# Optimization experiments

Measured on AMD Instinct MI355X. Metric: run time of the kernel, lower is better.

Reference implementation:

```python
import jax, jax.numpy as jnp
import numpy as np

K = 7           # kernel_size
GROUPS = 16     # channels // group_channels = 256 // 16
GC = 16         # group_channels
BN_EPS = 1e-5


def setup_inputs() -> dict:
    key = jax.random.key(0)
    ks = jax.random.split(key, 6)
    B, C, H, W = 4, 256, 64, 64
    cr = C // 4                      # reduction_ratio = 4
    k2g = K * K * GROUPS             # conv2 out channels = 784
    return {
        "feature_map": jax.random.normal(ks[0], (B, C, H, W), jnp.float32),
        "guide_map":   jax.random.normal(ks[1], (B, C, H, W), jnp.float32),
        "w1": jax.random.normal(ks[2], (cr, C), jnp.float32) * 0.05,
        "bn_gamma": jnp.ones((cr,), jnp.float32),
        "bn_beta":  jnp.zeros((cr,), jnp.float32),
        "bn_mean":  jax.random.normal(ks[3], (cr,), jnp.float32) * 0.1,
        "bn_var":   jax.random.uniform(ks[4], (cr,), jnp.float32, 0.5, 1.5),
        "w2": jax.random.normal(ks[5], (k2g, cr), jnp.float32) * 0.05,
        "b2": jnp.zeros((k2g,), jnp.float32),
    }


def reference(feature_map, guide_map, w1, bn_gamma, bn_beta, bn_mean, bn_var, w2, b2):
    b, c, h, w = feature_map.shape
    # conv1 (1x1) + BN (inference stats) + ReLU
    x = jnp.einsum("oc,bchw->bohw", w1, guide_map)
    inv = bn_gamma / jnp.sqrt(bn_var + BN_EPS)
    x = x * inv[None, :, None, None] + (bn_beta - bn_mean * inv)[None, :, None, None]
    x = jax.nn.relu(x)
    # conv2 (1x1): dynamic per-pixel kernel weights -> [b, groups, k^2, h, w]
    weight = jnp.einsum("oc,bchw->bohw", w2, x) + b2[None, :, None, None]
    weight = weight.reshape(b, GROUPS, K * K, h, w)
    # unfold feature_map (same padding, stride 1) -> [b, c, k^2, h, w]
    pad = (K - 1) // 2
    fp = jnp.pad(feature_map, ((0, 0), (0, 0), (pad, pad), (pad, pad)))
    patches = jnp.stack(
        [fp[:, :, i:i + h, j:j + w] for i in range(K) for j in range(K)], axis=2
    )
    patches = patches.reshape(b, GROUPS, GC, K * K, h, w)
    # dynamic weighted aggregation over kernel positions, then residual
    out = jnp.einsum("bgkhw,bgckhw->bgchw", weight, patches)
    return out.reshape(b, c, h, w) + feature_map
```

## Files before the change

### kernel.cpp

```cpp
#include <hip/hip_runtime.h>

#define BN_EPS 1e-5f

typedef __bf16 bf16_t;
typedef __bf16 bf16x8 __attribute__((ext_vector_type(8)));
typedef __bf16 bf16x4 __attribute__((ext_vector_type(4)));
typedef __bf16 bf16x2 __attribute__((ext_vector_type(2)));
typedef float  floatx4 __attribute__((ext_vector_type(4)));

#define MFMA16(a, b, c) __builtin_amdgcn_mfma_f32_16x16x32_bf16((a), (b), (c), 0, 0, 0)

#define XT_OFF  0
#define WG_OFF  0x200000
#define W1B_OFF 0x1A80000
#define W2B_OFF (0x1A80000 + 32768)
#define B1_OFF  (0x1A80000 + 32768 + 100352)

__global__ __launch_bounds__(256) void prep(
    const float* __restrict__ w1, const float* __restrict__ gamma,
    const float* __restrict__ beta, const float* __restrict__ mean,
    const float* __restrict__ var, const float* __restrict__ w2,
    bf16_t* __restrict__ w1b, bf16_t* __restrict__ w2b, float* __restrict__ bias1)
{
    const int idx = blockIdx.x * 256 + threadIdx.x;
    if (idx < 16384) {
        const int o = idx >> 8;
        const float inv = gamma[o] * rsqrtf(var[o] + BN_EPS);
        w1b[idx] = (bf16_t)(w1[idx] * inv);
        if (idx < 64) {
            const float iv = gamma[idx] * rsqrtf(var[idx] + BN_EPS);
            bias1[idx] = beta[idx] - mean[idx] * iv;
        }
    } else if (idx < 16384 + 50176) {
        const int j = idx - 16384;
        w2b[j] = (bf16_t)w2[j];
    }
}

#define GTP 264

__global__ __launch_bounds__(256) void conv1_k(
    const float* __restrict__ guide, const bf16_t* __restrict__ w1b,
    const float* __restrict__ bias1, bf16_t* __restrict__ xT)
{
    __shared__ __attribute__((aligned(16))) bf16_t gTs[64 * GTP];
    const int b = blockIdx.x >> 6, h = blockIdx.x & 63;
    const int t = threadIdx.x;

    const float* gsrc = guide + (size_t)b * 256 * 4096 + h * 64;
#pragma unroll
    for (int i = 0; i < 32; ++i) {
        const int idx = i * 256 + t;
        const int c2 = idx >> 6, p = idx & 63;
        const float g0 = gsrc[(size_t)(2 * c2) * 4096 + p];
        const float g1 = gsrc[(size_t)(2 * c2 + 1) * 4096 + p];
        bf16x2 pk; pk[0] = (bf16_t)g0; pk[1] = (bf16_t)g1;
        *(bf16x2*)&gTs[p * GTP + 2 * c2] = pk;
    }
    __syncthreads();

    const int wv = t >> 6, ln = t & 63, l15 = ln & 15, q = ln >> 4;
    floatx4 acc[4] = {};
    const bf16_t* ap = w1b + (wv * 16 + l15) * 256;
#pragma unroll
    for (int ks = 0; ks < 8; ++ks) {
        const bf16x8 a = *(const bf16x8*)(ap + ks * 32 + q * 8);
#pragma unroll
        for (int nt = 0; nt < 4; ++nt) {
            const bf16x8 bb = *(const bf16x8*)&gTs[(nt * 16 + l15) * GTP + ks * 32 + q * 8];
            acc[nt] = MFMA16(a, bb, acc[nt]);
        }
    }
    float bi[4];
#pragma unroll
    for (int j = 0; j < 4; ++j) bi[j] = bias1[wv * 16 + q * 4 + j];
#pragma unroll
    for (int nt = 0; nt < 4; ++nt) {
        const int p = nt * 16 + l15;
        bf16x4 v;
#pragma unroll
        for (int j = 0; j < 4; ++j) v[j] = (bf16_t)fmaxf(acc[nt][j] + bi[j], 0.f);
        *(bf16x4*)(xT + ((size_t)(b * 64 + h) * 64 + p) * 64 + wv * 16 + q * 4) = v;
    }
}

#define WTP 136

__global__ __launch_bounds__(256) void conv2_k(
    const bf16_t* __restrict__ xT, const bf16_t* __restrict__ w2b,
    const float* __restrict__ b2, bf16_t* __restrict__ wg)
{
    __shared__ __attribute__((aligned(16))) bf16_t wgt[64 * WTP];
    const int g = blockIdx.x & 15;
    const int bp0 = (blockIdx.x >> 4) * 128;
    const int t = threadIdx.x;
    const int wv = t >> 6, ln = t & 63, l15 = ln & 15, q = ln >> 4;

    floatx4 acc[4][2] = {};
    const bf16_t* brow = xT + (size_t)(bp0 + wv * 32) * 64;
#pragma unroll
    for (int ks = 0; ks < 2; ++ks) {
        bf16x8 bfr[2];
        bfr[0] = *(const bf16x8*)(brow + l15 * 64 + ks * 32 + q * 8);
        bfr[1] = *(const bf16x8*)(brow + (16 + l15) * 64 + ks * 32 + q * 8);
#pragma unroll
        for (int mt = 0; mt < 4; ++mt) {
            int row = mt * 16 + l15; if (row > 48) row = 48;
            const bf16x8 a = *(const bf16x8*)(w2b + (size_t)(g * 49 + row) * 64 + ks * 32 + q * 8);
            acc[mt][0] = MFMA16(a, bfr[0], acc[mt][0]);
            acc[mt][1] = MFMA16(a, bfr[1], acc[mt][1]);
        }
    }
#pragma unroll
    for (int mt = 0; mt < 4; ++mt) {
#pragma unroll
        for (int j = 0; j < 4; ++j) {
            const int k = mt * 16 + q * 4 + j;
            if (k < 49) {
                const float bias = b2[g * 49 + k];
                wgt[k * WTP + wv * 32 + l15]      = (bf16_t)(acc[mt][0][j] + bias);
                wgt[k * WTP + wv * 32 + 16 + l15] = (bf16_t)(acc[mt][1][j] + bias);
            }
        }
    }
    __syncthreads();
    for (int u = t; u < 784; u += 256) {
        const int k = u >> 4, c16 = u & 15;
        *(uint4*)(wg + (size_t)(g * 49 + k) * 16384 + bp0 + c16 * 8) =
            *(const uint4*)&wgt[k * WTP + c16 * 8];
    }
}

#define FSR 72
#define FSC 576
#define WGLP 136

__global__ __launch_bounds__(256) void agg_k(
    const bf16_t* __restrict__ wg, const float* __restrict__ feat,
    float* __restrict__ out)
{
    __shared__ __attribute__((aligned(16))) float  fs[16 * FSC];
    __shared__ __attribute__((aligned(16))) bf16_t wgl[49 * WGLP];

    const int g = blockIdx.x & 15;
    const int rest = blockIdx.x >> 4;
    const int b = rest >> 5, hp = rest & 31;
    const int h0 = hp * 2;
    const int t = threadIdx.x;

    for (int u = t; u < 784; u += 256) {
        const int k = u >> 4, c16 = u & 15;
        *(uint4*)&wgl[k * WGLP + c16 * 8] =
            *(const uint4*)(wg + (size_t)(g * 49 + k) * 16384 + b * 4096 + hp * 128 + c16 * 8);
    }
#pragma unroll
    for (int i = 0; i < 9; ++i) {
        const int u = i * 256 + t;
        const int c = u / 144, rem = u - c * 144;
        const int rr = rem / 18, qq = rem - rr * 18;
        const int hh = h0 - 3 + rr;
        float4 v = {0.f, 0.f, 0.f, 0.f};
        if (qq >= 1 && qq <= 16 && hh >= 0 && hh < 64)
            v = *(const float4*)(feat + ((size_t)(b * 256 + g * 16 + c) * 64 + hh) * 64 + (qq - 1) * 4);
        *(float4*)&fs[c * FSC + rr * FSR + qq * 4] = v;
    }
    __syncthreads();

    const int wq = t & 15, r = (t >> 4) & 1, cp = t >> 5;
    const int w0 = wq * 4;
    const int ch0 = cp * 2;

    float acc[2][4] = {};
#pragma unroll
    for (int di = 0; di < 7; ++di) {
        const int ri = r + di;
        float f0[12], f1[12];
        {
            const float* p0 = &fs[ch0 * FSC + ri * FSR + w0];
            const float* p1 = p0 + FSC;
#pragma unroll
            for (int qj = 0; qj < 3; ++qj) {
                const floatx4 a = *(const floatx4*)(p0 + qj * 4);
                const floatx4 bq = *(const floatx4*)(p1 + qj * 4);
#pragma unroll
                for (int j = 0; j < 4; ++j) { f0[qj * 4 + j] = a[j]; f1[qj * 4 + j] = bq[j]; }
            }
        }
        const bf16_t* wrow = &wgl[(di * 7) * WGLP + r * 64 + w0];
#pragma unroll
        for (int dj = 0; dj < 7; ++dj) {
            const bf16x4 wb = *(const bf16x4*)(wrow + dj * WGLP);
#pragma unroll
            for (int x = 0; x < 4; ++x) {
                const float wf = (float)wb[x];
                acc[0][x] = fmaf(wf, f0[x + dj + 1], acc[0][x]);
                acc[1][x] = fmaf(wf, f1[x + dj + 1], acc[1][x]);
            }
        }
    }

#pragma unroll
    for (int c = 0; c < 2; ++c) {
        const floatx4 res = *(const floatx4*)&fs[(ch0 + c) * FSC + (r + 3) * FSR + 4 + w0];
        const size_t ob = ((size_t)(b * 256 + g * 16 + ch0 + c) * 64 + h0 + r) * 64 + w0;
        float4 o;
        o.x = acc[c][0] + res[0]; o.y = acc[c][1] + res[1];
        o.z = acc[c][2] + res[2]; o.w = acc[c][3] + res[3];
        *(float4*)(out + ob) = o;
    }
}

extern "C" void kernel_launch(void* const* d_in, const int* in_sizes, int n_in,
                              void* d_out, int out_size, void* d_ws, size_t ws_size,
                              hipStream_t stream) {
    const float* feature = (const float*)d_in[0];
    const float* guide   = (const float*)d_in[1];
    const float* w1      = (const float*)d_in[2];
    const float* gamma   = (const float*)d_in[3];
    const float* beta    = (const float*)d_in[4];
    const float* mean    = (const float*)d_in[5];
    const float* var     = (const float*)d_in[6];
    const float* w2      = (const float*)d_in[7];
    const float* b2      = (const float*)d_in[8];
    float* out = (float*)d_out;

    char* ws = (char*)d_ws;
    bf16_t* xT    = (bf16_t*)(ws + XT_OFF);
    bf16_t* wg    = (bf16_t*)(ws + WG_OFF);
    bf16_t* w1b   = (bf16_t*)(ws + W1B_OFF);
    bf16_t* w2b   = (bf16_t*)(ws + W2B_OFF);
    float*  bias1 = (float*) (ws + B1_OFF);

    prep<<<260, 256, 0, stream>>>(w1, gamma, beta, mean, var, w2, w1b, w2b, bias1);
    conv1_k<<<256, 256, 0, stream>>>(guide, w1b, bias1, xT);
    conv2_k<<<2048, 256, 0, stream>>>(xT, w2b, b2, wg);
    agg_k<<<2048, 256, 0, stream>>>(wg, feature, out);
}
```

Measured before the change: 132.1 us.

## Fuse conv2 into aggregation kernel and fold weight prep into conv1

Removes the prep kernel by having conv1 fold BN scaling into w1 itself, converting to bf16 in shared memory. Conv2 is fused into the aggregation kernel: each block computes its 49x128 dynamic-weight tile with MFMA directly into LDS, so the large bf16 weight tensor is never written to or read from global memory. This cuts two launches and about 25MB of round-trip traffic. In exchange every conv1 block redoes the w1 conversion, agg blocks convert fp32 w2 on the fly, and LDS per block grows.

```diff
diff --git a/kernel.cpp b/kernel.cpp
--- a/kernel.cpp
+++ b/kernel.cpp
@@ -10,43 +10,32 @@
 
 #define MFMA16(a, b, c) __builtin_amdgcn_mfma_f32_16x16x32_bf16((a), (b), (c), 0, 0, 0)
 
-#define XT_OFF  0
-#define WG_OFF  0x200000
-#define W1B_OFF 0x1A80000
-#define W2B_OFF (0x1A80000 + 32768)
-#define B1_OFF  (0x1A80000 + 32768 + 100352)
-
-__global__ __launch_bounds__(256) void prep(
-    const float* __restrict__ w1, const float* __restrict__ gamma,
-    const float* __restrict__ beta, const float* __restrict__ mean,
-    const float* __restrict__ var, const float* __restrict__ w2,
-    bf16_t* __restrict__ w1b, bf16_t* __restrict__ w2b, float* __restrict__ bias1)
-{
-    const int idx = blockIdx.x * 256 + threadIdx.x;
-    if (idx < 16384) {
-        const int o = idx >> 8;
-        const float inv = gamma[o] * rsqrtf(var[o] + BN_EPS);
-        w1b[idx] = (bf16_t)(w1[idx] * inv);
-        if (idx < 64) {
-            const float iv = gamma[idx] * rsqrtf(var[idx] + BN_EPS);
-            bias1[idx] = beta[idx] - mean[idx] * iv;
-        }
-    } else if (idx < 16384 + 50176) {
-        const int j = idx - 16384;
-        w2b[j] = (bf16_t)w2[j];
-    }
-}
+#define XT_OFF 0
 
 #define GTP 264
+#define W1P 264
 
 __global__ __launch_bounds__(256) void conv1_k(
-    const float* __restrict__ guide, const bf16_t* __restrict__ w1b,
-    const float* __restrict__ bias1, bf16_t* __restrict__ xT)
+    const float* __restrict__ guide, const float* __restrict__ w1,
+    const float* __restrict__ gamma, const float* __restrict__ beta,
+    const float* __restrict__ mean,  const float* __restrict__ var,
+    bf16_t* __restrict__ xT)
 {
     __shared__ __attribute__((aligned(16))) bf16_t gTs[64 * GTP];
+    __shared__ __attribute__((aligned(16))) bf16_t w1s[64 * W1P];
     const int b = blockIdx.x >> 6, h = blockIdx.x & 63;
     const int t = threadIdx.x;
 
+#pragma unroll
+    for (int i = 0; i < 16; ++i) {
+        const int idx = i * 256 + t;
+        const int o = idx >> 6, cq = idx & 63;
+        const float inv = gamma[o] * rsqrtf(var[o] + BN_EPS);
+        const float4 v = *(const float4*)(w1 + o * 256 + cq * 4);
+        bf16_t* d = &w1s[o * W1P + cq * 4];
+        d[0] = (bf16_t)(v.x * inv); d[1] = (bf16_t)(v.y * inv);
+        d[2] = (bf16_t)(v.z * inv); d[3] = (bf16_t)(v.w * inv);
+    }
     const float* gsrc = guide + (size_t)b * 256 * 4096 + h * 64;
 #pragma unroll
     for (int i = 0; i < 32; ++i) {
@@ -61,7 +50,7 @@
 
     const int wv = t >> 6, ln = t & 63, l15 = ln & 15, q = ln >> 4;
     floatx4 acc[4] = {};
-    const bf16_t* ap = w1b + (wv * 16 + l15) * 256;
+    const bf16_t* ap = &w1s[(wv * 16 + l15) * W1P];
 #pragma unroll
     for (int ks = 0; ks < 8; ++ks) {
         const bf16x8 a = *(const bf16x8*)(ap + ks * 32 + q * 8);
@@ -73,7 +62,11 @@
     }
     float bi[4];
 #pragma unroll
-    for (int j = 0; j < 4; ++j) bi[j] = bias1[wv * 16 + q * 4 + j];
+    for (int j = 0; j < 4; ++j) {
+        const int o = wv * 16 + q * 4 + j;
+        const float iv = gamma[o] * rsqrtf(var[o] + BN_EPS);
+        bi[j] = beta[o] - mean[o] * iv;
+    }
 #pragma unroll
     for (int nt = 0; nt < 4; ++nt) {
         const int p = nt * 16 + l15;
@@ -84,75 +77,25 @@
     }
 }
 
-#define WTP 136
-
-__global__ __launch_bounds__(256) void conv2_k(
-    const bf16_t* __restrict__ xT, const bf16_t* __restrict__ w2b,
-    const float* __restrict__ b2, bf16_t* __restrict__ wg)
-{
-    __shared__ __attribute__((aligned(16))) bf16_t wgt[64 * WTP];
-    const int g = blockIdx.x & 15;
-    const int bp0 = (blockIdx.x >> 4) * 128;
-    const int t = threadIdx.x;
-    const int wv = t >> 6, ln = t & 63, l15 = ln & 15, q = ln >> 4;
-
-    floatx4 acc[4][2] = {};
-    const bf16_t* brow = xT + (size_t)(bp0 + wv * 32) * 64;
-#pragma unroll
-    for (int ks = 0; ks < 2; ++ks) {
-        bf16x8 bfr[2];
-        bfr[0] = *(const bf16x8*)(brow + l15 * 64 + ks * 32 + q * 8);
-        bfr[1] = *(const bf16x8*)(brow + (16 + l15) * 64 + ks * 32 + q * 8);
-#pragma unroll
-        for (int mt = 0; mt < 4; ++mt) {
-            int row = mt * 16 + l15; if (row > 48) row = 48;
-            const bf16x8 a = *(const bf16x8*)(w2b + (size_t)(g * 49 + row) * 64 + ks * 32 + q * 8);
-            acc[mt][0] = MFMA16(a, bfr[0], acc[mt][0]);
-            acc[mt][1] = MFMA16(a, bfr[1], acc[mt][1]);
-        }
-    }
-#pragma unroll
-    for (int mt = 0; mt < 4; ++mt) {
-#pragma unroll
-        for (int j = 0; j < 4; ++j) {
-            const int k = mt * 16 + q * 4 + j;
-            if (k < 49) {
-                const float bias = b2[g * 49 + k];
-                wgt[k * WTP + wv * 32 + l15]      = (bf16_t)(acc[mt][0][j] + bias);
-                wgt[k * WTP + wv * 32 + 16 + l15] = (bf16_t)(acc[mt][1][j] + bias);
-            }
-        }
-    }
-    __syncthreads();
-    for (int u = t; u < 784; u += 256) {
-        const int k = u >> 4, c16 = u & 15;
-        *(uint4*)(wg + (size_t)(g * 49 + k) * 16384 + bp0 + c16 * 8) =
-            *(const uint4*)&wgt[k * WTP + c16 * 8];
-    }
-}
-
 #define FSR 72
 #define FSC 576
-#define WGLP 136
-
-__global__ __launch_bounds__(256) void agg_k(
-    const bf16_t* __restrict__ wg, const float* __restrict__ feat,
+#define WGP 136
+
+__global__ __launch_bounds__(256) void fused_k(
+    const bf16_t* __restrict__ xT, const float* __restrict__ w2,
+    const float* __restrict__ b2,  const float* __restrict__ feat,
     float* __restrict__ out)
 {
     __shared__ __attribute__((aligned(16))) float  fs[16 * FSC];
-    __shared__ __attribute__((aligned(16))) bf16_t wgl[49 * WGLP];
+    __shared__ __attribute__((aligned(16))) bf16_t wgs[49 * WGP];
 
     const int g = blockIdx.x & 15;
     const int rest = blockIdx.x >> 4;
     const int b = rest >> 5, hp = rest & 31;
     const int h0 = hp * 2;
     const int t = threadIdx.x;
-
-    for (int u = t; u < 784; u += 256) {
-        const int k = u >> 4, c16 = u & 15;
-        *(uint4*)&wgl[k * WGLP + c16 * 8] =
-            *(const uint4*)(wg + (size_t)(g * 49 + k) * 16384 + b * 4096 + hp * 128 + c16 * 8);
-    }
+    const int wv = t >> 6, ln = t & 63, l15 = ln & 15, q = ln >> 4;
+
 #pragma unroll
     for (int i = 0; i < 9; ++i) {
         const int u = i * 256 + t;
@@ -164,6 +107,41 @@
             v = *(const float4*)(feat + ((size_t)(b * 256 + g * 16 + c) * 64 + hh) * 64 + (qq - 1) * 4);
         *(float4*)&fs[c * FSC + rr * FSR + qq * 4] = v;
     }
+
+    {
+        floatx4 acc[4][2] = {};
+        const bf16_t* brow = xT + ((size_t)(b * 64 + h0) * 64 + wv * 32) * 64;
+#pragma unroll
+        for (int ks = 0; ks < 2; ++ks) {
+            bf16x8 bfr[2];
+            bfr[0] = *(const bf16x8*)(brow + l15 * 64 + ks * 32 + q * 8);
+            bfr[1] = *(const bf16x8*)(brow + (16 + l15) * 64 + ks * 32 + q * 8);
+#pragma unroll
+            for (int mt = 0; mt < 4; ++mt) {
+                int row = mt * 16 + l15; if (row > 48) row = 48;
+                const float* wp = w2 + (size_t)(g * 49 + row) * 64 + ks * 32 + q * 8;
+                const float4 a0 = *(const float4*)(wp);
+                const float4 a1 = *(const float4*)(wp + 4);
+                bf16x8 a;
+                a[0] = (bf16_t)a0.x; a[1] = (bf16_t)a0.y; a[2] = (bf16_t)a0.z; a[3] = (bf16_t)a0.w;
+                a[4] = (bf16_t)a1.x; a[5] = (bf16_t)a1.y; a[6] = (bf16_t)a1.z; a[7] = (bf16_t)a1.w;
+                acc[mt][0] = MFMA16(a, bfr[0], acc[mt][0]);
+                acc[mt][1] = MFMA16(a, bfr[1], acc[mt][1]);
+            }
+        }
+#pragma unroll
+        for (int mt = 0; mt < 4; ++mt) {
+#pragma unroll
+            for (int j = 0; j < 4; ++j) {
+                const int k = mt * 16 + q * 4 + j;
+                if (k < 49) {
+                    const float bias = b2[g * 49 + k];
+                    wgs[k * WGP + wv * 32 + l15]      = (bf16_t)(acc[mt][0][j] + bias);
+                    wgs[k * WGP + wv * 32 + 16 + l15] = (bf16_t)(acc[mt][1][j] + bias);
+                }
+            }
+        }
+    }
     __syncthreads();
 
     const int wq = t & 15, r = (t >> 4) & 1, cp = t >> 5;
@@ -186,10 +164,10 @@
                 for (int j = 0; j < 4; ++j) { f0[qj * 4 + j] = a[j]; f1[qj * 4 + j] = bq[j]; }
             }
         }
-        const bf16_t* wrow = &wgl[(di * 7) * WGLP + r * 64 + w0];
+        const bf16_t* wrow = &wgs[(di * 7) * WGP + r * 64 + w0];
 #pragma unroll
         for (int dj = 0; dj < 7; ++dj) {
-            const bf16x4 wb = *(const bf16x4*)(wrow + dj * WGLP);
+            const bf16x4 wb = *(const bf16x4*)(wrow + dj * WGP);
 #pragma unroll
             for (int x = 0; x < 4; ++x) {
                 const float wf = (float)wb[x];
@@ -224,15 +202,8 @@
     const float* b2      = (const float*)d_in[8];
     float* out = (float*)d_out;
 
-    char* ws = (char*)d_ws;
-    bf16_t* xT    = (bf16_t*)(ws + XT_OFF);
-    bf16_t* wg    = (bf16_t*)(ws + WG_OFF);
-    bf16_t* w1b   = (bf16_t*)(ws + W1B_OFF);
-    bf16_t* w2b   = (bf16_t*)(ws + W2B_OFF);
-    float*  bias1 = (float*) (ws + B1_OFF);
-
-    prep<<<260, 256, 0, stream>>>(w1, gamma, beta, mean, var, w2, w1b, w2b, bias1);
-    conv1_k<<<256, 256, 0, stream>>>(guide, w1b, bias1, xT);
-    conv2_k<<<2048, 256, 0, stream>>>(xT, w2b, b2, wg);
-    agg_k<<<2048, 256, 0, stream>>>(wg, feature, out);
+    bf16_t* xT = (bf16_t*)((char*)d_ws + XT_OFF);
+
+    conv1_k<<<256, 256, 0, stream>>>(guide, w1, gamma, beta, mean, var, xT);
+    fused_k<<<2048, 256, 0, stream>>>(xT, w2, b2, feature, out);
 }
```

New measurement: 122.6 us. 7.2% less time.
